# Kernel optimization log

Measured on AMD Instinct MI355X. Metric: run time of the kernel, lower is better.

## Reference

```python
import jax, jax.numpy as jnp
import numpy as np

N, M, D = 8192, 65536, 512

def setup_inputs() -> dict:
    key = jax.random.key(0)
    k1, k2 = jax.random.split(key)
    embedding = jax.random.normal(k1, (N, D), dtype=jnp.float32)
    memory_bank = jax.random.normal(k2, (M, D), dtype=jnp.float32)
    return {"embedding": embedding, "memory_bank": memory_bank}

def reference(embedding, memory_bank):
    # torch.cdist(embedding, memory_bank, p=2.0) via the expansion
    x_sq = jnp.sum(embedding * embedding, axis=1, keepdims=True)        # [N, 1]
    m_sq = jnp.sum(memory_bank * memory_bank, axis=1)[None, :]          # [1, M]
    cross = embedding @ memory_bank.T                                    # [N, M]
    dist_sq = jnp.maximum(x_sq + m_sq - 2.0 * cross, 0.0)
    distances = jnp.sqrt(dist_sq)                                        # [N, M]
    # distances.topk(k=1, largest=False, dim=1) -> per-row min, kept dim
    patch_scores = jnp.min(distances, axis=1, keepdims=True)             # [N, 1]
    return patch_scores
```

## Files before the change

kernel.cpp:

```cpp
#include <hip/hip_runtime.h>
#include <stdint.h>

#define NROWS 8192
#define MROWS 65536
#define DDIM  512

#define BM 256
#define BN 256
#define CT 8
#define NKS 16
#define NT (CT * NKS)
#define NBUF 4
#define GRID_X ((NROWS / BM) * (MROWS / (BN * CT)))

typedef __attribute__((ext_vector_type(4))) float f32x4;
typedef __attribute__((ext_vector_type(8))) short short8;
typedef unsigned short ushort_t;
typedef unsigned int   uint_t;

__device__ __forceinline__ ushort_t f2bf(float x) {
    uint_t u = __float_as_uint(x);
    u += 0x7fffu + ((u >> 16) & 1u);
    return (ushort_t)(u >> 16);
}
__device__ __forceinline__ float bf2f(ushort_t b) {
    return __uint_as_float(((uint_t)b) << 16);
}

__device__ __forceinline__ void gll16(const void* g, void* l) {
    __builtin_amdgcn_global_load_lds((__attribute__((address_space(1))) void*)g,
                                     (__attribute__((address_space(3))) void*)l,
                                     16, 0, 0);
}

#define SBAR()   __builtin_amdgcn_s_barrier()
#define SCHED0() __builtin_amdgcn_sched_barrier(0)
#define LGKM0()  asm volatile("s_waitcnt lgkmcnt(0)" ::: "memory")

__global__ void init_minsq(uint_t* minsq) {
    int i = blockIdx.x * 256 + threadIdx.x;
    if (i < NROWS) minsq[i] = 0x7f800000u;
}

__global__ void convert_norms(const float* __restrict__ emb, const float* __restrict__ mem,
                              ushort_t* __restrict__ Abf, ushort_t* __restrict__ Bbf,
                              float* __restrict__ xsq, float* __restrict__ msq) {
    unsigned gid = blockIdx.x * 256 + threadIdx.x;
    unsigned row = gid >> 6;
    unsigned within = gid & 63u;
    unsigned seg = within >> 2, cc = within & 3u;
    int lane = threadIdx.x & 63;
    const float* src; ushort_t* dst; float* nrm; unsigned r;
    if (row < NROWS) { r = row;         src = emb + (size_t)r * DDIM; dst = Abf + (size_t)r * DDIM; nrm = xsq + r; }
    else             { r = row - NROWS; src = mem + (size_t)r * DDIM; dst = Bbf + (size_t)r * DDIM; nrm = msq + r; }
    unsigned scc = cc ^ ((r >> 1) & 3u);
    const float4* s4 = (const float4*)(src + seg * 32 + scc * 8);
    float4 a = s4[0], b = s4[1];
    ushort_t q[8];
    q[0]=f2bf(a.x); q[1]=f2bf(a.y); q[2]=f2bf(a.z); q[3]=f2bf(a.w);
    q[4]=f2bf(b.x); q[5]=f2bf(b.y); q[6]=f2bf(b.z); q[7]=f2bf(b.w);
    uint4 w;
    w.x = (uint_t)q[0] | ((uint_t)q[1] << 16);
    w.y = (uint_t)q[2] | ((uint_t)q[3] << 16);
    w.z = (uint_t)q[4] | ((uint_t)q[5] << 16);
    w.w = (uint_t)q[6] | ((uint_t)q[7] << 16);
    *(uint4*)(dst + seg * 32 + cc * 8) = w;
    float s = 0.f;
    #pragma unroll
    for (int i = 0; i < 8; ++i) { float v = bf2f(q[i]); s += v * v; }
    #pragma unroll
    for (int o = 1; o < 64; o <<= 1) s += __shfl_xor(s, o);
    if (lane == 0) *nrm = s;
}

__global__ __launch_bounds__(512, 2) void gemm256_min(
    const ushort_t* __restrict__ Abf, const ushort_t* __restrict__ Bbf,
    const float* __restrict__ xsq, const float* __restrict__ msq,
    uint_t* __restrict__ minsq)
{
    __shared__ alignas(16) ushort_t As[NBUF][256 * 32];
    __shared__ alignas(16) ushort_t Bs[NBUF][256 * 32];
    __shared__ float Ms[BN * CT];

    const int tid  = threadIdx.x;
    const int lane = tid & 63;
    const int wave = tid >> 6;
    const int wm   = wave >> 2;
    const int wn   = wave & 3;
    const int laneRow = lane & 15;
    const int laneK   = lane >> 4;

    unsigned wg  = blockIdx.x;
    unsigned swz = (wg & 7u) * (GRID_X / 8) + (wg >> 3);
    const unsigned rt = swz & 31u;
    const unsigned cg = swz >> 5;
    const size_t r0    = (size_t)rt * BM;
    const size_t cbase = (size_t)cg * (BN * CT);

    const int chunk = ((laneK ^ ((laneRow >> 1) & 3)) << 4);
    int offA[8], offB[4];
    #pragma unroll
    for (int m = 0; m < 8; ++m) offA[m] = (wm * 128 + m * 16 + laneRow) * 64 + chunk;
    #pragma unroll
    for (int n = 0; n < 4; ++n) offB[n] = (wn * 64 + n * 16 + laneRow) * 64 + chunk;

    const int rowoff = wave * 16 + (lane >> 2);
    const int inrow  = (lane & 3) * 16;
    const char* Agb = (const char*)Abf + (r0 + rowoff) * 1024 + inrow;
    const char* Bgb = (const char*)Bbf + (cbase + rowoff) * 1024 + inrow;

    f32x4 acc[8][4];
    float runmin[8][4];
    #pragma unroll
    for (int m = 0; m < 8; ++m)
        #pragma unroll
        for (int n = 0; n < 4; ++n) { acc[m][n] = (f32x4)0.f; runmin[m][n] = 3.0e38f; }

    #pragma unroll
    for (int i = 0; i < 4; ++i) {
        int idx = i * 512 + tid;
        Ms[idx] = msq[cbase + idx];
    }
    asm volatile("s_waitcnt vmcnt(0)" ::: "memory");
    SCHED0();

    #pragma unroll
    for (int s = 0; s < 3; ++s) {
        char* lB = (char*)&Bs[s][0] + wave * 1024;
        char* lA = (char*)&As[s][0] + wave * 1024;
        gll16(Bgb + s * 64, lB); gll16(Bgb + s * 64 + 131072, lB + 8192);
        gll16(Agb + s * 64, lA); gll16(Agb + s * 64 + 131072, lA + 8192);
    }
    asm volatile("s_waitcnt vmcnt(8)" ::: "memory");
    SBAR();

    for (int t = 0; t < NT; ++t) {
        const char* rA = (const char*)&As[t & 3][0];
        const char* rB = (const char*)&Bs[t & 3][0];
        const bool stg = (t + 3) < NT;
        const int s3  = t + 3;
        const int ks3 = s3 & 15;
        const int ct3 = s3 >> 4;
        const char* gA3 = Agb + ks3 * 64;
        const char* gB3 = Bgb + (size_t)ct3 * 256 * 1024 + ks3 * 64;
        char* lA3 = (char*)&As[s3 & 3][0] + wave * 1024;
        char* lB3 = (char*)&Bs[s3 & 3][0] + wave * 1024;

        short8 a0[4], a1[4], b[4];

        #pragma unroll
        for (int n = 0; n < 4; ++n) b[n]  = *(const short8*)(rB + offB[n]);
        #pragma unroll
        for (int m = 0; m < 4; ++m) a0[m] = *(const short8*)(rA + offA[m]);
        if (stg) { gll16(gB3, lB3); gll16(gB3 + 131072, lB3 + 8192); }
        SBAR();
        LGKM0(); SCHED0();
        __builtin_amdgcn_s_setprio(1);
        #pragma unroll
        for (int m = 0; m < 4; ++m)
            #pragma unroll
            for (int n = 0; n < 4; ++n)
                acc[m][n] = __builtin_amdgcn_mfma_f32_16x16x32_bf16(a0[m], b[n], acc[m][n], 0, 0, 0);
        __builtin_amdgcn_s_setprio(0);
        SBAR();

        #pragma unroll
        for (int m = 0; m < 4; ++m) a1[m] = *(const short8*)(rA + offA[m + 4]);
        if (stg) { gll16(gA3, lA3); gll16(gA3 + 131072, lA3 + 8192); }
        SBAR();
        LGKM0(); SCHED0();
        __builtin_amdgcn_s_setprio(1);
        #pragma unroll
        for (int m = 0; m < 4; ++m)
            #pragma unroll
            for (int n = 0; n < 4; ++n)
                acc[m + 4][n] = __builtin_amdgcn_mfma_f32_16x16x32_bf16(a1[m], b[n], acc[m + 4][n], 0, 0, 0);
        __builtin_amdgcn_s_setprio(0);
        if (t < NT - 3)       { asm volatile("s_waitcnt vmcnt(8)" ::: "memory"); SBAR(); }
        else if (t == NT - 3) { asm volatile("s_waitcnt vmcnt(4)" ::: "memory"); SBAR(); }
        else if (t == NT - 2) { asm volatile("s_waitcnt vmcnt(0)" ::: "memory"); SBAR(); }

        if ((t & 15) == 15) {
            const int ctf = t >> 4;
            float mc[4];
            #pragma unroll
            for (int n = 0; n < 4; ++n) mc[n] = Ms[ctf * 256 + wn * 64 + n * 16 + laneRow];
            #pragma unroll
            for (int m = 0; m < 8; ++m)
                #pragma unroll
                for (int n = 0; n < 4; ++n) {
                    #pragma unroll
                    for (int j = 0; j < 4; ++j)
                        runmin[m][j] = fminf(runmin[m][j], fmaf(-2.f, acc[m][n][j], mc[n]));
                    acc[m][n] = (f32x4)0.f;
                }
        }
    }

    #pragma unroll
    for (int m = 0; m < 8; ++m)
        #pragma unroll
        for (int j = 0; j < 4; ++j) {
            float v = runmin[m][j];
            v = fminf(v, __shfl_xor(v, 1));
            v = fminf(v, __shfl_xor(v, 2));
            v = fminf(v, __shfl_xor(v, 4));
            v = fminf(v, __shfl_xor(v, 8));
            if ((lane & 15) == 0) {
                int grow = (int)r0 + wm * 128 + m * 16 + laneK * 4 + j;
                float d2 = fmaxf(v + xsq[grow], 0.f);
                atomicMin(&minsq[grow], __float_as_uint(d2));
            }
        }
}

__global__ void finish_kernel(const uint_t* __restrict__ minsq, float* __restrict__ out) {
    int i = blockIdx.x * 256 + threadIdx.x;
    if (i < NROWS) out[i] = sqrtf(__uint_as_float(minsq[i]));
}

__global__ void norms_kernel(const float* __restrict__ emb, const float* __restrict__ mem,
                             float* __restrict__ xsq, float* __restrict__ msq) {
    int row  = blockIdx.x * 4 + (threadIdx.x >> 6);
    int lane = threadIdx.x & 63;
    const float* src; float* dst;
    if (row < NROWS) { src = emb + (size_t)row * DDIM;           dst = xsq + row; }
    else             { src = mem + (size_t)(row - NROWS) * DDIM; dst = msq + (row - NROWS); }
    float4 f0 = *(const float4*)(src + lane * 8);
    float4 f1 = *(const float4*)(src + lane * 8 + 4);
    float s = 0.f, v;
    v = bf2f(f2bf(f0.x)); s += v*v;  v = bf2f(f2bf(f0.y)); s += v*v;
    v = bf2f(f2bf(f0.z)); s += v*v;  v = bf2f(f2bf(f0.w)); s += v*v;
    v = bf2f(f2bf(f1.x)); s += v*v;  v = bf2f(f2bf(f1.y)); s += v*v;
    v = bf2f(f2bf(f1.z)); s += v*v;  v = bf2f(f2bf(f1.w)); s += v*v;
    #pragma unroll
    for (int o = 1; o < 64; o <<= 1) s += __shfl_xor(s, o);
    if (lane == 0) *dst = s;
}

__device__ __forceinline__ void fb_stage_load(const float* __restrict__ emb,
                                              const float* __restrict__ mem,
                                              size_t r0, size_t c0, int ks,
                                              float4* ra, float4* rb, int tid) {
    #pragma unroll
    for (int p = 0; p < 4; ++p) {
        int row = p * 32 + (tid >> 3);
        int c   = (tid & 7) * 8;
        const float* sa = emb + (r0 + row) * DDIM + ks * 64 + c;
        const float* sb = mem + (c0 + row) * DDIM + ks * 64 + c;
        ra[2*p]   = *(const float4*)sa;  ra[2*p+1] = *(const float4*)(sa + 4);
        rb[2*p]   = *(const float4*)sb;  rb[2*p+1] = *(const float4*)(sb + 4);
    }
}
__device__ __forceinline__ void fb_stage_write(ushort_t* Ab, ushort_t* Bb,
                                               const float4* ra, const float4* rb, int tid) {
    #pragma unroll
    for (int p = 0; p < 4; ++p) {
        int row = p * 32 + (tid >> 3);
        int ccs = (tid & 7) ^ (row & 7);
        uint4 wa, wb;
        wa.x = (uint_t)f2bf(ra[2*p].x)   | ((uint_t)f2bf(ra[2*p].y)   << 16);
        wa.y = (uint_t)f2bf(ra[2*p].z)   | ((uint_t)f2bf(ra[2*p].w)   << 16);
        wa.z = (uint_t)f2bf(ra[2*p+1].x) | ((uint_t)f2bf(ra[2*p+1].y) << 16);
        wa.w = (uint_t)f2bf(ra[2*p+1].z) | ((uint_t)f2bf(ra[2*p+1].w) << 16);
        wb.x = (uint_t)f2bf(rb[2*p].x)   | ((uint_t)f2bf(rb[2*p].y)   << 16);
        wb.y = (uint_t)f2bf(rb[2*p].z)   | ((uint_t)f2bf(rb[2*p].w)   << 16);
        wb.z = (uint_t)f2bf(rb[2*p+1].x) | ((uint_t)f2bf(rb[2*p+1].y) << 16);
        wb.w = (uint_t)f2bf(rb[2*p+1].z) | ((uint_t)f2bf(rb[2*p+1].w) << 16);
        *(uint4*)&Ab[row * 64 + ccs * 8] = wa;
        *(uint4*)&Bb[row * 64 + ccs * 8] = wb;
    }
}

__global__ __launch_bounds__(256, 2) void gemm_min_fb(
    const float* __restrict__ emb, const float* __restrict__ mem,
    const float* __restrict__ xsq, const float* __restrict__ msq,
    uint_t* __restrict__ minsq)
{
    __shared__ alignas(16) ushort_t Ab[128 * 64];
    __shared__ alignas(16) ushort_t Bb[128 * 64];
    const int tid = threadIdx.x, lane = tid & 63, wave = tid >> 6;
    const int wm = wave >> 1, wn = wave & 1;
    unsigned wg = blockIdx.x;
    unsigned swz = (wg & 7u) * (2048 / 8) + (wg >> 3);
    const unsigned rt = swz & 63u, cgf = swz >> 6;
    const size_t r0 = (size_t)rt * 128;
    float runmin[4][4];
    #pragma unroll
    for (int m = 0; m < 4; ++m)
        #pragma unroll
        for (int j = 0; j < 4; ++j) runmin[m][j] = 3.0e38f;
    float4 ra[8], rb[8];
    for (int ctf = 0; ctf < 16; ++ctf) {
        const size_t c0 = ((size_t)cgf * 16 + ctf) * 128;
        f32x4 acc[4][4] = {};
        fb_stage_load(emb, mem, r0, c0, 0, ra, rb, tid);
        for (int ks = 0; ks < 8; ++ks) {
            __syncthreads();
            fb_stage_write(Ab, Bb, ra, rb, tid);
            if (ks + 1 < 8) fb_stage_load(emb, mem, r0, c0, ks + 1, ra, rb, tid);
            __syncthreads();
            #pragma unroll
            for (int kk = 0; kk < 2; ++kk) {
                short8 af[4], bfm[4];
                #pragma unroll
                for (int m = 0; m < 4; ++m) {
                    int r = wm * 64 + m * 16 + (lane & 15);
                    int c = ((kk * 4 + (lane >> 4)) ^ (r & 7)) * 8;
                    af[m] = *(const short8*)&Ab[r * 64 + c];
                }
                #pragma unroll
                for (int n = 0; n < 4; ++n) {
                    int r = wn * 64 + n * 16 + (lane & 15);
                    int c = ((kk * 4 + (lane >> 4)) ^ (r & 7)) * 8;
                    bfm[n] = *(const short8*)&Bb[r * 64 + c];
                }
                #pragma unroll
                for (int m = 0; m < 4; ++m)
                    #pragma unroll
                    for (int n = 0; n < 4; ++n)
                        acc[m][n] = __builtin_amdgcn_mfma_f32_16x16x32_bf16(af[m], bfm[n], acc[m][n], 0, 0, 0);
            }
        }
        float mcf[4];
        #pragma unroll
        for (int n = 0; n < 4; ++n) mcf[n] = msq[c0 + wn * 64 + n * 16 + (lane & 15)];
        #pragma unroll
        for (int m = 0; m < 4; ++m)
            #pragma unroll
            for (int n = 0; n < 4; ++n)
                #pragma unroll
                for (int j = 0; j < 4; ++j)
                    runmin[m][j] = fminf(runmin[m][j], fmaf(-2.f, acc[m][n][j], mcf[n]));
    }
    #pragma unroll
    for (int m = 0; m < 4; ++m)
        #pragma unroll
        for (int j = 0; j < 4; ++j) {
            float v = runmin[m][j];
            v = fminf(v, __shfl_xor(v, 1));
            v = fminf(v, __shfl_xor(v, 2));
            v = fminf(v, __shfl_xor(v, 4));
            v = fminf(v, __shfl_xor(v, 8));
            if ((lane & 15) == 0) {
                int grow = (int)r0 + wm * 64 + m * 16 + (lane >> 4) * 4 + j;
                float d2 = fmaxf(v + xsq[grow], 0.f);
                atomicMin(&minsq[grow], __float_as_uint(d2));
            }
        }
}

extern "C" void kernel_launch(void* const* d_in, const int* in_sizes, int n_in,
                              void* d_out, int out_size, void* d_ws, size_t ws_size,
                              hipStream_t stream) {
    const float* emb = (const float*)d_in[0];
    const float* mem = (const float*)d_in[1];
    float* out = (float*)d_out;

    char* ws = (char*)d_ws;
    float*  xsq   = (float*)ws;
    float*  msq   = (float*)(ws + 32768);
    uint_t* minsq = (uint_t*)(ws + 32768 + 262144);
    ushort_t* Abf = (ushort_t*)(ws + 327680);
    ushort_t* Bbf = Abf + (size_t)NROWS * DDIM;
    const size_t NEED = 327680 + ((size_t)NROWS + MROWS) * DDIM * 2;

    init_minsq<<<(NROWS + 255) / 256, 256, 0, stream>>>(minsq);
    if (ws_size >= NEED) {
        convert_norms<<<((NROWS + MROWS) * 64) / 256, 256, 0, stream>>>(emb, mem, Abf, Bbf, xsq, msq);
        gemm256_min<<<GRID_X, 512, 0, stream>>>(Abf, Bbf, xsq, msq, minsq);
    } else {
        norms_kernel<<<(NROWS + MROWS) / 4, 256, 0, stream>>>(emb, mem, xsq, msq);
        gemm_min_fb<<<2048, 256, 0, stream>>>(emb, mem, xsq, msq, minsq);
    }
    finish_kernel<<<(NROWS + 255) / 256, 256, 0, stream>>>(minsq, out);
}
```

Before: 584.6 us.

## Restructure LDS pipeline into K=64 steps with staggered A/B prefetch

Replaces the 4-slot ring of K=32 stages with a double-buffered layout in which each step covers two K=32 halves. A is prefetched one step ahead and B two steps ahead, with an unrolled pair of steps so buffer parity is known at compile time. The aim is to cut per-step index arithmetic and to rebalance load and MFMA interleaving. It keeps the same LDS footprint, adds more vmcnt waits per step, and has a tighter prefetch distance for A, which risks exposing load latency.

```diff
diff --git a/kernel.cpp b/kernel.cpp
--- a/kernel.cpp
+++ b/kernel.cpp
@@ -8,9 +8,8 @@
 #define BM 256
 #define BN 256
 #define CT 8
-#define NKS 16
-#define NT (CT * NKS)
-#define NBUF 4
+#define KS_PER_CT 8
+#define NT (CT * KS_PER_CT)
 #define GRID_X ((NROWS / BM) * (MROWS / (BN * CT)))
 
 typedef __attribute__((ext_vector_type(4))) float f32x4;
@@ -78,8 +77,8 @@
     const float* __restrict__ xsq, const float* __restrict__ msq,
     uint_t* __restrict__ minsq)
 {
-    __shared__ alignas(16) ushort_t As[NBUF][256 * 32];
-    __shared__ alignas(16) ushort_t Bs[NBUF][256 * 32];
+    __shared__ alignas(16) ushort_t As[2][2][256 * 32];
+    __shared__ alignas(16) ushort_t Bs[2][2][256 * 32];
     __shared__ float Ms[BN * CT];
 
     const int tid  = threadIdx.x;
@@ -124,78 +123,110 @@
     asm volatile("s_waitcnt vmcnt(0)" ::: "memory");
     SCHED0();
 
-    #pragma unroll
-    for (int s = 0; s < 3; ++s) {
-        char* lB = (char*)&Bs[s][0] + wave * 1024;
-        char* lA = (char*)&As[s][0] + wave * 1024;
-        gll16(Bgb + s * 64, lB); gll16(Bgb + s * 64 + 131072, lB + 8192);
-        gll16(Agb + s * 64, lA); gll16(Agb + s * 64 + 131072, lA + 8192);
+    {
+        char* b00 = (char*)&Bs[0][0][0] + wave * 1024;
+        char* a00 = (char*)&As[0][0][0] + wave * 1024;
+        char* b01 = (char*)&Bs[0][1][0] + wave * 1024;
+        char* a01 = (char*)&As[0][1][0] + wave * 1024;
+        char* b10 = (char*)&Bs[1][0][0] + wave * 1024;
+        char* b11 = (char*)&Bs[1][1][0] + wave * 1024;
+        gll16(Bgb,       b00); gll16(Bgb + 131072,       b00 + 8192);
+        gll16(Agb,       a00); gll16(Agb + 131072,       a00 + 8192);
+        gll16(Bgb + 64,  b01); gll16(Bgb + 64 + 131072,  b01 + 8192);
+        gll16(Agb + 64,  a01); gll16(Agb + 64 + 131072,  a01 + 8192);
+        gll16(Bgb + 128, b10); gll16(Bgb + 128 + 131072, b10 + 8192);
+        gll16(Bgb + 192, b11); gll16(Bgb + 192 + 131072, b11 + 8192);
     }
     asm volatile("s_waitcnt vmcnt(8)" ::: "memory");
     SBAR();
 
-    for (int t = 0; t < NT; ++t) {
-        const char* rA = (const char*)&As[t & 3][0];
-        const char* rB = (const char*)&Bs[t & 3][0];
-        const bool stg = (t + 3) < NT;
-        const int s3  = t + 3;
-        const int ks3 = s3 & 15;
-        const int ct3 = s3 >> 4;
-        const char* gA3 = Agb + ks3 * 64;
-        const char* gB3 = Bgb + (size_t)ct3 * 256 * 1024 + ks3 * 64;
-        char* lA3 = (char*)&As[s3 & 3][0] + wave * 1024;
-        char* lB3 = (char*)&Bs[s3 & 3][0] + wave * 1024;
-
-        short8 a0[4], a1[4], b[4];
-
-        #pragma unroll
-        for (int n = 0; n < 4; ++n) b[n]  = *(const short8*)(rB + offB[n]);
-        #pragma unroll
-        for (int m = 0; m < 4; ++m) a0[m] = *(const short8*)(rA + offA[m]);
-        if (stg) { gll16(gB3, lB3); gll16(gB3 + 131072, lB3 + 8192); }
-        SBAR();
-        LGKM0(); SCHED0();
-        __builtin_amdgcn_s_setprio(1);
-        #pragma unroll
-        for (int m = 0; m < 4; ++m)
-            #pragma unroll
-            for (int n = 0; n < 4; ++n)
-                acc[m][n] = __builtin_amdgcn_mfma_f32_16x16x32_bf16(a0[m], b[n], acc[m][n], 0, 0, 0);
-        __builtin_amdgcn_s_setprio(0);
-        SBAR();
-
-        #pragma unroll
-        for (int m = 0; m < 4; ++m) a1[m] = *(const short8*)(rA + offA[m + 4]);
-        if (stg) { gll16(gA3, lA3); gll16(gA3 + 131072, lA3 + 8192); }
-        SBAR();
-        LGKM0(); SCHED0();
-        __builtin_amdgcn_s_setprio(1);
-        #pragma unroll
-        for (int m = 0; m < 4; ++m)
-            #pragma unroll
-            for (int n = 0; n < 4; ++n)
-                acc[m + 4][n] = __builtin_amdgcn_mfma_f32_16x16x32_bf16(a1[m], b[n], acc[m + 4][n], 0, 0, 0);
-        __builtin_amdgcn_s_setprio(0);
-        if (t < NT - 3)       { asm volatile("s_waitcnt vmcnt(8)" ::: "memory"); SBAR(); }
-        else if (t == NT - 3) { asm volatile("s_waitcnt vmcnt(4)" ::: "memory"); SBAR(); }
-        else if (t == NT - 2) { asm volatile("s_waitcnt vmcnt(0)" ::: "memory"); SBAR(); }
-
-        if ((t & 15) == 15) {
-            const int ctf = t >> 4;
-            float mc[4];
-            #pragma unroll
-            for (int n = 0; n < 4; ++n) mc[n] = Ms[ctf * 256 + wn * 64 + n * 16 + laneRow];
-            #pragma unroll
-            for (int m = 0; m < 8; ++m)
-                #pragma unroll
-                for (int n = 0; n < 4; ++n) {
-                    #pragma unroll
-                    for (int j = 0; j < 4; ++j)
-                        runmin[m][j] = fminf(runmin[m][j], fmaf(-2.f, acc[m][n][j], mc[n]));
-                    acc[m][n] = (f32x4)0.f;
-                }
-        }
-    }
+#define GSTEP(T, PAR)                                                               \
+    {                                                                               \
+        const bool deep = (T) < NT - 3;                                             \
+        const bool stgA = (T) + 1 < NT;                                             \
+        const bool stgB = (T) + 2 < NT;                                             \
+        const char* gA1 = Agb + (size_t)(((T) + 1) & 7) * 128;                      \
+        const char* gB2 = Bgb + (size_t)(((T) + 2) >> 3) * 262144                   \
+                              + (size_t)(((T) + 2) & 7) * 128;                      \
+        const char* rA0 = (const char*)&As[PAR][0][0];                              \
+        const char* rA1 = (const char*)&As[PAR][1][0];                              \
+        const char* rB0 = (const char*)&Bs[PAR][0][0];                              \
+        const char* rB1 = (const char*)&Bs[PAR][1][0];                              \
+        char* sA0 = (char*)&As[(PAR) ^ 1][0][0] + wave * 1024;                      \
+        char* sA1 = (char*)&As[(PAR) ^ 1][1][0] + wave * 1024;                      \
+        char* sB0 = (char*)&Bs[PAR][0][0] + wave * 1024;                            \
+        char* sB1 = (char*)&Bs[PAR][1][0] + wave * 1024;                            \
+        short8 a0[4], a1v[4], b[4];                                                 \
+                                                                 \
+        _Pragma("unroll") for (int n = 0; n < 4; ++n) b[n]  = *(const short8*)(rB0 + offB[n]); \
+        _Pragma("unroll") for (int m = 0; m < 4; ++m) a0[m] = *(const short8*)(rA0 + offA[m]); \
+        if (stgA) { gll16(gA1, sA0); gll16(gA1 + 131072, sA0 + 8192); }             \
+        SBAR();                                                                     \
+        LGKM0(); SCHED0();                                                          \
+        __builtin_amdgcn_s_setprio(1);                                              \
+        _Pragma("unroll") for (int m = 0; m < 4; ++m)                               \
+            _Pragma("unroll") for (int n = 0; n < 4; ++n)                           \
+                acc[m][n] = __builtin_amdgcn_mfma_f32_16x16x32_bf16(a0[m], b[n], acc[m][n], 0, 0, 0); \
+        __builtin_amdgcn_s_setprio(0);                                              \
+        SBAR();                                                                     \
+                                                                 \
+        _Pragma("unroll") for (int m = 0; m < 4; ++m) a1v[m] = *(const short8*)(rA0 + offA[m + 4]); \
+        if (stgB) { gll16(gB2, sB0); gll16(gB2 + 131072, sB0 + 8192); }             \
+        SBAR();                                                                     \
+        LGKM0(); SCHED0();                                                          \
+        __builtin_amdgcn_s_setprio(1);                                              \
+        _Pragma("unroll") for (int m = 0; m < 4; ++m)                               \
+            _Pragma("unroll") for (int n = 0; n < 4; ++n)                           \
+                acc[m + 4][n] = __builtin_amdgcn_mfma_f32_16x16x32_bf16(a1v[m], b[n], acc[m + 4][n], 0, 0, 0); \
+        __builtin_amdgcn_s_setprio(0);                                              \
+        if (deep) { asm volatile("s_waitcnt vmcnt(6)" ::: "memory"); }              \
+        else      { asm volatile("s_waitcnt vmcnt(0)" ::: "memory"); }              \
+        SCHED0(); SBAR();                                                           \
+                                                                 \
+        _Pragma("unroll") for (int n = 0; n < 4; ++n) b[n]  = *(const short8*)(rB1 + offB[n]); \
+        _Pragma("unroll") for (int m = 0; m < 4; ++m) a0[m] = *(const short8*)(rA1 + offA[m]); \
+        if (stgA) { gll16(gA1 + 64, sA1); gll16(gA1 + 64 + 131072, sA1 + 8192); }   \
+        SBAR();                                                                     \
+        LGKM0(); SCHED0();                                                          \
+        __builtin_amdgcn_s_setprio(1);                                              \
+        _Pragma("unroll") for (int m = 0; m < 4; ++m)                               \
+            _Pragma("unroll") for (int n = 0; n < 4; ++n)                           \
+                acc[m][n] = __builtin_amdgcn_mfma_f32_16x16x32_bf16(a0[m], b[n], acc[m][n], 0, 0, 0); \
+        __builtin_amdgcn_s_setprio(0);                                              \
+        SBAR();                                                                     \
+                                                                 \
+        _Pragma("unroll") for (int m = 0; m < 4; ++m) a1v[m] = *(const short8*)(rA1 + offA[m + 4]); \
+        if (stgB) { gll16(gB2 + 64, sB1); gll16(gB2 + 64 + 131072, sB1 + 8192); }   \
+        SBAR();                                                                     \
+        LGKM0(); SCHED0();                                                          \
+        __builtin_amdgcn_s_setprio(1);                                              \
+        _Pragma("unroll") for (int m = 0; m < 4; ++m)                               \
+            _Pragma("unroll") for (int n = 0; n < 4; ++n)                           \
+                acc[m + 4][n] = __builtin_amdgcn_mfma_f32_16x16x32_bf16(a1v[m], b[n], acc[m + 4][n], 0, 0, 0); \
+        __builtin_amdgcn_s_setprio(0);                                              \
+        if (deep) { asm volatile("s_waitcnt vmcnt(6)" ::: "memory"); }              \
+        else      { asm volatile("s_waitcnt vmcnt(0)" ::: "memory"); }              \
+        SCHED0(); SBAR();                                                           \
+                                                  \
+        if (((T) & 7) == 7) {                                                       \
+            const int ctf = (T) >> 3;                                               \
+            float mc[4];                                                            \
+            _Pragma("unroll") for (int n = 0; n < 4; ++n)                           \
+                mc[n] = Ms[ctf * 256 + wn * 64 + n * 16 + laneRow];                 \
+            _Pragma("unroll") for (int m = 0; m < 8; ++m)                           \
+                _Pragma("unroll") for (int n = 0; n < 4; ++n) {                     \
+                    _Pragma("unroll") for (int j = 0; j < 4; ++j)                   \
+                        runmin[m][j] = fminf(runmin[m][j], fmaf(-2.f, acc[m][n][j], mc[n])); \
+                    acc[m][n] = (f32x4)0.f;                                         \
+                }                                                                   \
+        }                                                                           \
+    }
+
+    for (int t = 0; t < NT; t += 2) {
+        GSTEP(t, 0);
+        GSTEP(t + 1, 1);
+    }
+#undef GSTEP
 
     #pragma unroll
     for (int m = 0; m < 8; ++m)
```

Result: no change. 592.5 us (+1.3%).
